# Kernel tuning notes

Hardware: AMD Instinct MI355X
Metric: run time of the kernel (lower is better)

The kernel has to match this reference:

```python
import jax, jax.numpy as jnp
import numpy as np

N, F_IN, F_OUT, HEADS = 4096, 128, 64, 4


def setup_inputs() -> dict:
    key = jax.random.key(0)
    k1, k2, k3, k4, k5 = jax.random.split(key, 5)
    X = jax.random.normal(k1, (N, F_IN), dtype=jnp.float32)
    A = jax.random.randint(k2, (N, N), 0, 2, dtype=jnp.int32)
    # zero the diagonal: the torch loop always prepends the self node, so the
    # adjacency must not also contain it (would duplicate the self term).
    A = A * (1 - jnp.eye(N, dtype=jnp.int32))
    # per-head Linear(F_IN, F_OUT) weights/bias and Linear(2*F_OUT, 1, bias=False)
    W = jax.random.normal(k3, (HEADS, F_OUT, F_IN), dtype=jnp.float32) / np.sqrt(F_IN)
    b = jax.random.normal(k4, (HEADS, F_OUT), dtype=jnp.float32) * 0.02
    att = jax.random.normal(k5, (HEADS, 2 * F_OUT), dtype=jnp.float32) / np.sqrt(2 * F_OUT)
    return {"X": X, "A": A, "W": W, "b": b, "att": att}


def reference(X, A, W, b, att):
    # H[h, n, o] = line_h(X)
    H = jnp.einsum('nf,hof->hno', X, W) + b[:, None, :]
    f_out = W.shape[1]
    a_src, a_dst = att[:, :f_out], att[:, f_out:]
    # score e_ij = leaky_relu(a_src.H_i + a_dst.H_j)
    s = jnp.einsum('hno,ho->hn', H, a_src)  # query-side term (xi_bar expanded)
    d = jnp.einsum('hno,ho->hn', H, a_dst)  # neighbor-side term
    e = jax.nn.leaky_relu(s[:, :, None] + d[:, None, :])  # [H, N, N]
    # neighbor set = {self} U {j : A_ij != 0}
    mask = (A > 0) | jnp.eye(A.shape[0], dtype=bool)
    e = jnp.where(mask[None], e, -jnp.inf)
    alpha = jax.nn.softmax(e, axis=-1)  # segment softmax per node row
    # weighted sum per head, then mean over heads (sum / head in the original)
    out = jnp.einsum('hnm,hmo->no', alpha, H) / W.shape[0]
    return out  # [N, F_OUT]
```

## Files before the change

kernel.cpp:

```cpp
#include <hip/hip_runtime.h>
#include <hip/hip_bf16.h>


#define NN 4096
#define FIN 128
#define FOUT 64
#define NH 4

typedef __attribute__((ext_vector_type(8))) short bf16x8;
typedef __attribute__((ext_vector_type(4))) float f32x4;
typedef __attribute__((ext_vector_type(4))) unsigned int u32x4;

__device__ __forceinline__ unsigned short f32_bf16(float f) {
    unsigned u = __builtin_bit_cast(unsigned, f);
    u += 0x7fffu + ((u >> 16) & 1u);
    return (unsigned short)(u >> 16);
}

__global__ __launch_bounds__(256) void pack_bits(
    const int* __restrict__ A, unsigned long long* __restrict__ Abits)
{
    const int row  = blockIdx.x;
    const int lane = threadIdx.x & 63;
    const int wv   = threadIdx.x >> 6;
    const int* arow = A + (size_t)row * NN;
    #pragma unroll 4
    for (int c = 0; c < 16; ++c) {
        const int col = c * 256 + wv * 64 + lane;
        unsigned long long m = __ballot(__builtin_nontemporal_load(&arow[col]) > 0);
        if (lane == 0) Abits[(size_t)row * 64 + c * 4 + wv] = m;
    }
}

__global__ __launch_bounds__(256) void gat_prep(
    const float* __restrict__ X, const float* __restrict__ W,
    const float* __restrict__ b, const float* __restrict__ att,
    unsigned short* __restrict__ HbfT, float* __restrict__ Hrow,
    float* __restrict__ s_out, float* __restrict__ d_out,
    float* __restrict__ es_g, float* __restrict__ es2_g,
    float* __restrict__ ed_g, float* __restrict__ ed2_g)
{
    const int rb = blockIdx.x;
    const int h  = blockIdx.y;
    const int n0 = rb * 32;
    const int t  = threadIdx.x;

    __shared__ float Xl[32][132];
    __shared__ float Wt[128][68];

    for (int g = t; g < 32 * 32; g += 256) {
        int row = g >> 5, c4 = g & 31;
        float4 v = *(const float4*)&X[(size_t)(n0 + row) * FIN + c4 * 4];
        *(float4*)&Xl[row][c4 * 4] = v;
    }
    for (int g = t; g < 64 * 32; g += 256) {
        int o = g >> 5, c4 = g & 31;
        float4 v = *(const float4*)&W[((size_t)h * FOUT + o) * FIN + c4 * 4];
        Wt[c4 * 4 + 0][o] = v.x; Wt[c4 * 4 + 1][o] = v.y;
        Wt[c4 * 4 + 2][o] = v.z; Wt[c4 * 4 + 3][o] = v.w;
    }
    __syncthreads();

    const int rg = t >> 4;
    const int og = t & 15;
    float acc[2][4] = {};

    #pragma unroll 4
    for (int f4 = 0; f4 < 32; ++f4) {
        float xv[2][4], wv[4][4];
        #pragma unroll
        for (int i = 0; i < 2; ++i) {
            float4 tmp = *(const float4*)&Xl[rg * 2 + i][f4 * 4];
            xv[i][0] = tmp.x; xv[i][1] = tmp.y; xv[i][2] = tmp.z; xv[i][3] = tmp.w;
        }
        #pragma unroll
        for (int k = 0; k < 4; ++k) {
            float4 tmp = *(const float4*)&Wt[f4 * 4 + k][og * 4];
            wv[k][0] = tmp.x; wv[k][1] = tmp.y; wv[k][2] = tmp.z; wv[k][3] = tmp.w;
        }
        #pragma unroll
        for (int i = 0; i < 2; ++i)
            #pragma unroll
            for (int k = 0; k < 4; ++k)
                #pragma unroll
                for (int jj = 0; jj < 4; ++jj)
                    acc[i][jj] = fmaf(xv[i][k], wv[k][jj], acc[i][jj]);
    }

    float bb[4], as_[4], ad_[4];
    #pragma unroll
    for (int jj = 0; jj < 4; ++jj) {
        bb[jj]  = b[h * FOUT + og * 4 + jj];
        as_[jj] = att[h * 2 * FOUT + og * 4 + jj];
        ad_[jj] = att[h * 2 * FOUT + FOUT + og * 4 + jj];
    }
    #pragma unroll
    for (int i = 0; i < 2; ++i)
        #pragma unroll
        for (int jj = 0; jj < 4; ++jj)
            acc[i][jj] += bb[jj];

    float sp[2] = {0.f, 0.f}, dp[2] = {0.f, 0.f};
    #pragma unroll
    for (int i = 0; i < 2; ++i)
        #pragma unroll
        for (int jj = 0; jj < 4; ++jj) {
            sp[i] = fmaf(acc[i][jj], as_[jj], sp[i]);
            dp[i] = fmaf(acc[i][jj], ad_[jj], dp[i]);
        }
    #pragma unroll
    for (int off = 1; off < 16; off <<= 1) {
        #pragma unroll
        for (int i = 0; i < 2; ++i) {
            sp[i] += __shfl_xor(sp[i], off);
            dp[i] += __shfl_xor(dp[i], off);
        }
    }
    if (og == 0) {
        #pragma unroll
        for (int i = 0; i < 2; ++i) {
            int nn = n0 + rg * 2 + i;
            s_out[h * NN + nn]  = sp[i];
            d_out[h * NN + nn]  = dp[i];
            es_g [h * NN + nn]  = __expf(sp[i]);
            es2_g[h * NN + nn]  = __expf(0.01f * sp[i]);
            ed_g [h * NN + nn]  = __expf(dp[i]);
            ed2_g[h * NN + nn]  = __expf(0.01f * dp[i]);
        }
    }

    #pragma unroll
    for (int i = 0; i < 2; ++i) {
        float4 v = make_float4(acc[i][0], acc[i][1], acc[i][2], acc[i][3]);
        *(float4*)&Hrow[((size_t)h * NN + n0 + rg * 2 + i) * FOUT + og * 4] = v;
    }
    #pragma unroll
    for (int jj = 0; jj < 4; ++jj) {
        int o = og * 4 + jj;
        ushort2 p;
        p.x = f32_bf16(acc[0][jj]);
        p.y = f32_bf16(acc[1][jj]);
        *(ushort2*)&HbfT[((size_t)h * FOUT + o) * NN + n0 + rg * 2] = p;
    }
}

__global__ __launch_bounds__(512, 4) void gat_main(
    const unsigned* __restrict__ Abits, const unsigned short* __restrict__ HbfT,
    const float* __restrict__ s_g, const float* __restrict__ d_g,
    const float* __restrict__ es_g, const float* __restrict__ es2_g,
    const float* __restrict__ ed_g, const float* __restrict__ ed2_g,
    const float* __restrict__ Hrow, float* __restrict__ outH)
{
    const int id   = blockIdx.x;
    const int h    = id & 3;
    const int tile = id >> 2;
    const int n0   = tile * 32;
    const int tid  = threadIdx.x;
    const int w    = tid >> 6;
    const int lane = tid & 63;
    const int r    = lane & 15;
    const int q    = lane >> 4;
    const int qs   = q * 8;
    const int rg   = w & 1;
    const int kg   = w >> 1;

    __shared__ __align__(16) unsigned short Hlds[2][64][128];
    __shared__ unsigned bits_lds[2][32 * 5];
    __shared__ float red[6][16][68];
    __shared__ float redl[6][16];

    const int nrow = n0 + rg * 16 + r;
    const float es  = es_g [h * NN + nrow];
    const float es2 = es2_g[h * NN + nrow];

    const int mb       = (kg * 4 + q) ^ r;
    const int bits_idx = (rg * 16 + r) * 5 + kg;

    const int so = tid >> 4;
    const int sc = tid & 15;
    const unsigned short* srcA = HbfT + ((size_t)(h * FOUT) + so)      * NN + sc * 8;
    const unsigned short* srcB = HbfT + ((size_t)(h * FOUT) + so + 32) * NN + sc * 8;
    const int offA = so * 128        + (sc ^ (so & 15)) * 8;
    const int offB = (so + 32) * 128 + (sc ^ (so & 15)) * 8;
    const int brow = tid >> 2, bwd = tid & 3;
    const unsigned* srcBits = Abits + (size_t)(n0 + brow) * 128 + bwd;

    const float* edh  = ed_g  + h * NN + kg * 32 + qs;
    const float* ed2h = ed2_g + h * NN + kg * 32 + qs;

    bf16x8 ones;
    #pragma unroll
    for (int i = 0; i < 8; ++i) ones[i] = (short)0x3F80;

    f32x4 acc0 = {0,0,0,0}, acc1 = {0,0,0,0}, acc2 = {0,0,0,0},
          acc3 = {0,0,0,0}, accl = {0,0,0,0};

    bf16x8 stA, stB;
    unsigned stBits = 0;

    stA = *(const bf16x8*)&srcA[0];
    stB = *(const bf16x8*)&srcB[0];
    {
        unsigned short* hw = &Hlds[0][0][0];
        *(bf16x8*)(hw + offA) = stA;
        *(bf16x8*)(hw + offB) = stB;
        if (tid < 128) bits_lds[0][brow * 5 + bwd] = srcBits[0];
    }
    __syncthreads();

    for (int ch = 0; ch < 32; ++ch) {
        const int buf = ch & 1;
        const unsigned short* hb = buf ? &Hlds[1][0][0] : &Hlds[0][0][0];
        const unsigned*       bl = buf ? bits_lds[1]    : bits_lds[0];

        if (ch < 31) {
            stA = *(const bf16x8*)&srcA[(ch + 1) * 128];
            stB = *(const bf16x8*)&srcB[(ch + 1) * 128];
            if (tid < 128) stBits = srcBits[(ch + 1) * 4];
        }

        const unsigned bits8 = bl[bits_idx] >> qs;
        const int cb = ch * 128;
        const float4 e0 = *(const float4*)&edh [cb];
        const float4 e1 = *(const float4*)&edh [cb + 4];
        const float4 g0 = *(const float4*)&ed2h[cb];
        const float4 g1 = *(const float4*)&ed2h[cb + 4];
        const float edv [8] = {e0.x, e0.y, e0.z, e0.w, e1.x, e1.y, e1.z, e1.w};
        const float ed2v[8] = {g0.x, g0.y, g0.z, g0.w, g1.x, g1.y, g1.z, g1.w};

        u32x4 afu;
        #pragma unroll
        for (int p = 0; p < 4; ++p) {
            const int j0 = 2 * p, j1 = 2 * p + 1;
            float wa = (bits8 & (1u << j0))
                     ? fmaxf(es * edv[j0], es2 * ed2v[j0]) : 0.0f;
            float wb = (bits8 & (1u << j1))
                     ? fmaxf(es * edv[j1], es2 * ed2v[j1]) : 0.0f;
            __hip_bfloat162 pk = __float22bfloat162_rn(make_float2(wa, wb));
            unsigned u;
            __builtin_memcpy(&u, &pk, sizeof(u));
            afu[p] = u;
        }
        const bf16x8 af = __builtin_bit_cast(bf16x8, afu);

        const bf16x8 b0 = *(const bf16x8*)&hb[(r     ) * 128 + mb * 8];
        const bf16x8 b1 = *(const bf16x8*)&hb[(r + 16) * 128 + mb * 8];
        const bf16x8 b2 = *(const bf16x8*)&hb[(r + 32) * 128 + mb * 8];
        const bf16x8 b3 = *(const bf16x8*)&hb[(r + 48) * 128 + mb * 8];

        acc0 = __builtin_amdgcn_mfma_f32_16x16x32_bf16(af, b0,   acc0, 0, 0, 0);
        acc1 = __builtin_amdgcn_mfma_f32_16x16x32_bf16(af, b1,   acc1, 0, 0, 0);
        acc2 = __builtin_amdgcn_mfma_f32_16x16x32_bf16(af, b2,   acc2, 0, 0, 0);
        acc3 = __builtin_amdgcn_mfma_f32_16x16x32_bf16(af, b3,   acc3, 0, 0, 0);
        accl = __builtin_amdgcn_mfma_f32_16x16x32_bf16(af, ones, accl, 0, 0, 0);

        if (ch < 31) {
            unsigned short* hw = buf ? &Hlds[0][0][0] : &Hlds[1][0][0];
            *(bf16x8*)(hw + offA) = stA;
            *(bf16x8*)(hw + offB) = stB;
            if (tid < 128) (buf ? bits_lds[0] : bits_lds[1])[brow * 5 + bwd] = stBits;
        }
        __syncthreads();
    }

    if (kg > 0) {
        const int widx = (kg - 1) * 2 + rg;
        #pragma unroll
        for (int reg = 0; reg < 4; ++reg) {
            const int rr = q * 4 + reg;
            red[widx][rr][ 0 + r] = acc0[reg];
            red[widx][rr][16 + r] = acc1[reg];
            red[widx][rr][32 + r] = acc2[reg];
            red[widx][rr][48 + r] = acc3[reg];
        }
        if (r == 0) {
            #pragma unroll
            for (int reg = 0; reg < 4; ++reg)
                redl[widx][q * 4 + reg] = accl[reg];
        }
    }
    __syncthreads();
    if (kg == 0) {
        #pragma unroll
        for (int kk = 0; kk < 3; ++kk) {
            const int widx = kk * 2 + rg;
            #pragma unroll
            for (int reg = 0; reg < 4; ++reg) {
                const int rr = q * 4 + reg;
                acc0[reg] += red[widx][rr][ 0 + r];
                acc1[reg] += red[widx][rr][16 + r];
                acc2[reg] += red[widx][rr][32 + r];
                acc3[reg] += red[widx][rr][48 + r];
                accl[reg] += redl[widx][rr];
            }
        }
        #pragma unroll
        for (int reg = 0; reg < 4; ++reg) {
            const int rr  = q * 4 + reg;
            const int nn2 = n0 + rg * 16 + rr;
            const float tt = s_g[h * NN + nn2] + d_g[h * NN + nn2];
            const float wd = __expf(fmaxf(tt, 0.01f * tt));
            const float inv = 0.25f / (accl[reg] + wd);
            const float* hr = &Hrow[((size_t)h * NN + nn2) * FOUT];
            float*       ob = &outH[((size_t)h * NN + nn2) * FOUT];
            ob[ 0 + r] = (acc0[reg] + wd * hr[ 0 + r]) * inv;
            ob[16 + r] = (acc1[reg] + wd * hr[16 + r]) * inv;
            ob[32 + r] = (acc2[reg] + wd * hr[32 + r]) * inv;
            ob[48 + r] = (acc3[reg] + wd * hr[48 + r]) * inv;
        }
    }
}

__global__ __launch_bounds__(256) void gat_fin(
    const float* __restrict__ outH, float* __restrict__ out)
{
    const int i = blockIdx.x * 256 + threadIdx.x;
    const f32x4* p = (const f32x4*)outH;
    f32x4 v0 = __builtin_nontemporal_load(p + i);
    f32x4 v1 = __builtin_nontemporal_load(p + i +  65536);
    f32x4 v2 = __builtin_nontemporal_load(p + i + 131072);
    f32x4 v3 = __builtin_nontemporal_load(p + i + 196608);
    f32x4 s = (v0 + v1) + (v2 + v3);
    *((f32x4*)out + i) = s;
}

extern "C" void kernel_launch(void* const* d_in, const int* in_sizes, int n_in,
                              void* d_out, int out_size, void* d_ws, size_t ws_size,
                              hipStream_t stream) {
    const float* X   = (const float*)d_in[0];
    const int*   A   = (const int*)  d_in[1];
    const float* W   = (const float*)d_in[2];
    const float* b   = (const float*)d_in[3];
    const float* att = (const float*)d_in[4];
    float* out = (float*)d_out;

    char* ws = (char*)d_ws;
    unsigned short* HbfT = (unsigned short*)ws;
    size_t off = (size_t)NH * FOUT * NN * 2;
    float* s_buf   = (float*)(ws + off);  off += (size_t)NH * NN * 4;
    float* d_buf   = (float*)(ws + off);  off += (size_t)NH * NN * 4;
    float* es_buf  = (float*)(ws + off);  off += (size_t)NH * NN * 4;
    float* es2_buf = (float*)(ws + off);  off += (size_t)NH * NN * 4;
    float* ed_buf  = (float*)(ws + off);  off += (size_t)NH * NN * 4;
    float* ed2_buf = (float*)(ws + off);  off += (size_t)NH * NN * 4;
    unsigned long long* Abits = (unsigned long long*)(ws + off);
    off += (size_t)NN * 64 * 8;
    float* Hrow   = (float*)(ws + off);
    off += (size_t)NH * NN * FOUT * 4;
    float* outH   = (float*)(ws + off);
    off += (size_t)NH * NN * FOUT * 4;

    pack_bits<<<NN, 256, 0, stream>>>(A, Abits);
    gat_prep<<<dim3(128, 4), 256, 0, stream>>>(X, W, b, att, HbfT, Hrow,
                                               s_buf, d_buf,
                                               es_buf, es2_buf, ed_buf, ed2_buf);
    gat_main<<<512, 512, 0, stream>>>((const unsigned*)Abits, HbfT,
                                      s_buf, d_buf,
                                      es_buf, es2_buf, ed_buf, ed2_buf,
                                      Hrow, outH);
    gat_fin<<<256, 256, 0, stream>>>(outH, out);
}
```

Before: 166.7 us.

## Split neighbor axis across all waves and load H fragments directly from global

The main attention kernel now gives each block 16 query rows instead of 32 and launches twice as many blocks. Each of the 8 waves takes a contiguous 512-column slice of the neighbor range. The waves load bf16 H fragments, adjacency bits and ed values straight from global memory, replacing the LDS double-buffered staging and the per-chunk __syncthreads. Partial sums from all 8 waves are reduced through shared memory at the end. This drops the barrier and LDS traffic, but each H tile is now read from global or L2 by fewer rows, and the reduction grows to 7 partials.

```diff
diff --git a/kernel.cpp b/kernel.cpp
--- a/kernel.cpp
+++ b/kernel.cpp
@@ -153,40 +153,28 @@
 {
     const int id   = blockIdx.x;
     const int h    = id & 3;
-    const int tile = id >> 2;
-    const int n0   = tile * 32;
+    const int rgp  = id >> 2;
+    const int n0   = rgp * 16;
     const int tid  = threadIdx.x;
     const int w    = tid >> 6;
     const int lane = tid & 63;
     const int r    = lane & 15;
     const int q    = lane >> 4;
     const int qs   = q * 8;
-    const int rg   = w & 1;
-    const int kg   = w >> 1;
-
-    __shared__ __align__(16) unsigned short Hlds[2][64][128];
-    __shared__ unsigned bits_lds[2][32 * 5];
-    __shared__ float red[6][16][68];
-    __shared__ float redl[6][16];
-
-    const int nrow = n0 + rg * 16 + r;
+    const int wc0  = w * 512;
+
+    __shared__ float red[7][16][68];
+    __shared__ float redl[7][16];
+
+    const int nrow = n0 + r;
     const float es  = es_g [h * NN + nrow];
     const float es2 = es2_g[h * NN + nrow];
 
-    const int mb       = (kg * 4 + q) ^ r;
-    const int bits_idx = (rg * 16 + r) * 5 + kg;
-
-    const int so = tid >> 4;
-    const int sc = tid & 15;
-    const unsigned short* srcA = HbfT + ((size_t)(h * FOUT) + so)      * NN + sc * 8;
-    const unsigned short* srcB = HbfT + ((size_t)(h * FOUT) + so + 32) * NN + sc * 8;
-    const int offA = so * 128        + (sc ^ (so & 15)) * 8;
-    const int offB = (so + 32) * 128 + (sc ^ (so & 15)) * 8;
-    const int brow = tid >> 2, bwd = tid & 3;
-    const unsigned* srcBits = Abits + (size_t)(n0 + brow) * 128 + bwd;
-
-    const float* edh  = ed_g  + h * NN + kg * 32 + qs;
-    const float* ed2h = ed2_g + h * NN + kg * 32 + qs;
+    const unsigned* bitsPtr = Abits + (size_t)nrow * 128 + (wc0 >> 5);
+    const float* edh  = ed_g  + h * NN + wc0 + qs;
+    const float* ed2h = ed2_g + h * NN + wc0 + qs;
+    const unsigned short* srcH =
+        HbfT + ((size_t)(h * FOUT + r) * NN) + wc0 + q * 8;
 
     bf16x8 ones;
     #pragma unroll
@@ -195,36 +183,20 @@
     f32x4 acc0 = {0,0,0,0}, acc1 = {0,0,0,0}, acc2 = {0,0,0,0},
           acc3 = {0,0,0,0}, accl = {0,0,0,0};
 
-    bf16x8 stA, stB;
-    unsigned stBits = 0;
-
-    stA = *(const bf16x8*)&srcA[0];
-    stB = *(const bf16x8*)&srcB[0];
-    {
-        unsigned short* hw = &Hlds[0][0][0];
-        *(bf16x8*)(hw + offA) = stA;
-        *(bf16x8*)(hw + offB) = stB;
-        if (tid < 128) bits_lds[0][brow * 5 + bwd] = srcBits[0];
-    }
-    __syncthreads();
-
-    for (int ch = 0; ch < 32; ++ch) {
-        const int buf = ch & 1;
-        const unsigned short* hb = buf ? &Hlds[1][0][0] : &Hlds[0][0][0];
-        const unsigned*       bl = buf ? bits_lds[1]    : bits_lds[0];
-
-        if (ch < 31) {
-            stA = *(const bf16x8*)&srcA[(ch + 1) * 128];
-            stB = *(const bf16x8*)&srcB[(ch + 1) * 128];
-            if (tid < 128) stBits = srcBits[(ch + 1) * 4];
-        }
-
-        const unsigned bits8 = bl[bits_idx] >> qs;
-        const int cb = ch * 128;
+    #pragma unroll 2
+    for (int t = 0; t < 16; ++t) {
+        const int cb = t * 32;
+        const unsigned bitsW = bitsPtr[t];
         const float4 e0 = *(const float4*)&edh [cb];
         const float4 e1 = *(const float4*)&edh [cb + 4];
         const float4 g0 = *(const float4*)&ed2h[cb];
         const float4 g1 = *(const float4*)&ed2h[cb + 4];
+        const bf16x8 b0 = *(const bf16x8*)&srcH[cb];
+        const bf16x8 b1 = *(const bf16x8*)&srcH[16 * NN + cb];
+        const bf16x8 b2 = *(const bf16x8*)&srcH[32 * NN + cb];
+        const bf16x8 b3 = *(const bf16x8*)&srcH[48 * NN + cb];
+
+        const unsigned bits8 = bitsW >> qs;
         const float edv [8] = {e0.x, e0.y, e0.z, e0.w, e1.x, e1.y, e1.z, e1.w};
         const float ed2v[8] = {g0.x, g0.y, g0.z, g0.w, g1.x, g1.y, g1.z, g1.w};
 
@@ -243,61 +215,46 @@
         }
         const bf16x8 af = __builtin_bit_cast(bf16x8, afu);
 
-        const bf16x8 b0 = *(const bf16x8*)&hb[(r     ) * 128 + mb * 8];
-        const bf16x8 b1 = *(const bf16x8*)&hb[(r + 16) * 128 + mb * 8];
-        const bf16x8 b2 = *(const bf16x8*)&hb[(r + 32) * 128 + mb * 8];
-        const bf16x8 b3 = *(const bf16x8*)&hb[(r + 48) * 128 + mb * 8];
-
         acc0 = __builtin_amdgcn_mfma_f32_16x16x32_bf16(af, b0,   acc0, 0, 0, 0);
         acc1 = __builtin_amdgcn_mfma_f32_16x16x32_bf16(af, b1,   acc1, 0, 0, 0);
         acc2 = __builtin_amdgcn_mfma_f32_16x16x32_bf16(af, b2,   acc2, 0, 0, 0);
         acc3 = __builtin_amdgcn_mfma_f32_16x16x32_bf16(af, b3,   acc3, 0, 0, 0);
         accl = __builtin_amdgcn_mfma_f32_16x16x32_bf16(af, ones, accl, 0, 0, 0);
-
-        if (ch < 31) {
-            unsigned short* hw = buf ? &Hlds[0][0][0] : &Hlds[1][0][0];
-            *(bf16x8*)(hw + offA) = stA;
-            *(bf16x8*)(hw + offB) = stB;
-            if (tid < 128) (buf ? bits_lds[0] : bits_lds[1])[brow * 5 + bwd] = stBits;
-        }
-        __syncthreads();
-    }
-
-    if (kg > 0) {
-        const int widx = (kg - 1) * 2 + rg;
+    }
+
+    if (w > 0) {
         #pragma unroll
         for (int reg = 0; reg < 4; ++reg) {
             const int rr = q * 4 + reg;
-            red[widx][rr][ 0 + r] = acc0[reg];
-            red[widx][rr][16 + r] = acc1[reg];
-            red[widx][rr][32 + r] = acc2[reg];
-            red[widx][rr][48 + r] = acc3[reg];
+            red[w - 1][rr][ 0 + r] = acc0[reg];
+            red[w - 1][rr][16 + r] = acc1[reg];
+            red[w - 1][rr][32 + r] = acc2[reg];
+            red[w - 1][rr][48 + r] = acc3[reg];
         }
         if (r == 0) {
             #pragma unroll
             for (int reg = 0; reg < 4; ++reg)
-                redl[widx][q * 4 + reg] = accl[reg];
+                redl[w - 1][q * 4 + reg] = accl[reg];
         }
     }
     __syncthreads();
-    if (kg == 0) {
-        #pragma unroll
-        for (int kk = 0; kk < 3; ++kk) {
-            const int widx = kk * 2 + rg;
+    if (w == 0) {
+        #pragma unroll
+        for (int kk = 0; kk < 7; ++kk) {
             #pragma unroll
             for (int reg = 0; reg < 4; ++reg) {
                 const int rr = q * 4 + reg;
-                acc0[reg] += red[widx][rr][ 0 + r];
-                acc1[reg] += red[widx][rr][16 + r];
-                acc2[reg] += red[widx][rr][32 + r];
-                acc3[reg] += red[widx][rr][48 + r];
-                accl[reg] += redl[widx][rr];
+                acc0[reg] += red[kk][rr][ 0 + r];
+                acc1[reg] += red[kk][rr][16 + r];
+                acc2[reg] += red[kk][rr][32 + r];
+                acc3[reg] += red[kk][rr][48 + r];
+                accl[reg] += redl[kk][rr];
             }
         }
         #pragma unroll
         for (int reg = 0; reg < 4; ++reg) {
             const int rr  = q * 4 + reg;
-            const int nn2 = n0 + rg * 16 + rr;
+            const int nn2 = n0 + rr;
             const float tt = s_g[h * NN + nn2] + d_g[h * NN + nn2];
             const float wd = __expf(fmaxf(tt, 0.01f * tt));
             const float inv = 0.25f / (accl[reg] + wd);
@@ -354,9 +311,9 @@
     gat_prep<<<dim3(128, 4), 256, 0, stream>>>(X, W, b, att, HbfT, Hrow,
                                                s_buf, d_buf,
                                                es_buf, es2_buf, ed_buf, ed2_buf);
-    gat_main<<<512, 512, 0, stream>>>((const unsigned*)Abits, HbfT,
-                                      s_buf, d_buf,
-                                      es_buf, es2_buf, ed_buf, ed2_buf,
-                                      Hrow, outH);
+    gat_main<<<1024, 512, 0, stream>>>((const unsigned*)Abits, HbfT,
+                                       s_buf, d_buf,
+                                       es_buf, es2_buf, ed_buf, ed2_buf,
+                                       Hrow, outH);
     gat_fin<<<256, 256, 0, stream>>>(outH, out);
 }
```

Result: slower. 219.6 us (+31.8%).
